# Performance work log

Hardware: AMD Instinct MI355X
Metric: run time of the kernel (lower is better)

Reference implementation:

```python
import jax, jax.numpy as jnp
import numpy as np

MASK_VALUE = -1000000.0  # matches torch sequence_mask fill value


def setup_inputs() -> dict:
    key = jax.random.key(0)
    k1, k2, k3, k4 = jax.random.split(key, 4)
    B, Tq, Tk, d = 16, 2048, 2048, 128
    queries = jax.random.normal(k1, (B, Tq, d), dtype=jnp.float32)
    keys = jax.random.normal(k2, (B, Tk, d), dtype=jnp.float32)
    values = jax.random.normal(k3, (B, Tk, d), dtype=jnp.float32)
    valid_lens = jax.random.randint(k4, (B, Tq), 0, Tk, dtype=jnp.int64)
    return {"queries": queries, "keys": keys, "values": values,
            "valid_lens": valid_lens}


def reference(queries, keys, values, valid_lens):
    d = queries.shape[-1]
    Tk = keys.shape[1]
    # scores: [B, Tq, Tk]
    scores = jnp.einsum('bqd,bkd->bqk', queries, keys) / jnp.sqrt(
        jnp.asarray(d, dtype=queries.dtype))
    # per-row length mask: position k is valid iff k < valid_lens[b, q]
    mask = jnp.arange(Tk)[None, None, :] < valid_lens[:, :, None]
    scores = jnp.where(mask, scores, jnp.asarray(MASK_VALUE, scores.dtype))
    attn = jax.nn.softmax(scores, axis=-1)
    # dropout p=0.0 -> identity
    return jnp.einsum('bqk,bkd->bqd', attn, values)
```

## Files before the change

### kernel.cpp

```cpp
#include <hip/hip_runtime.h>
#include <stdint.h>
#include <math.h>

#define NB 16
#define TQ 2048
#define TK 2048
#define DH 128

#define QK_STR 136
#define VT_STR 72
#define P_STR  72

typedef __attribute__((ext_vector_type(8))) short bf16x8;
typedef __attribute__((ext_vector_type(4))) float f32x4;
typedef __attribute__((ext_vector_type(8))) unsigned short u16x8;

__device__ __forceinline__ unsigned short f2b(float f) {
  union { float f; uint32_t u; } v; v.f = f;
  uint32_t u = v.u;
  return (unsigned short)((u + 0x7fffu + ((u >> 16) & 1u)) >> 16);
}

__device__ __forceinline__ u16x8 cvt8(const float* p) {
  const f32x4 a = *(const f32x4*)p;
  const f32x4 b = *(const f32x4*)(p + 4);
  u16x8 o;
#pragma unroll
  for (int j = 0; j < 4; ++j) { o[j] = f2b(a[j]); o[4 + j] = f2b(b[j]); }
  return o;
}

__global__ __launch_bounds__(256) void prep_kernel(const float* __restrict__ K,
                                                   const float* __restrict__ V,
                                                   unsigned short* __restrict__ Kb,
                                                   unsigned short* __restrict__ Vt) {
  __shared__ alignas(16) unsigned short tile[64][136];
  const int t = threadIdx.x;
  const int b = blockIdx.y;
  const int k0 = blockIdx.x * 64;

  const float* Ks = K + ((size_t)b * TK + k0) * DH;
  unsigned short* Kd = Kb + ((size_t)b * TK + k0) * DH;
#pragma unroll
  for (int i = 0; i < 4; ++i) {
    const int row = i * 16 + (t >> 4);
    const int c0 = (t & 15) * 8;
    *(u16x8*)(Kd + (size_t)row * DH + c0) = cvt8(Ks + (size_t)row * DH + c0);
  }
  const float* Vs = V + ((size_t)b * TK + k0) * DH;
#pragma unroll
  for (int i = 0; i < 4; ++i) {
    const int row = i * 16 + (t >> 4);
    const int c0 = (t & 15) * 8;
    *(u16x8*)(&tile[row][c0]) = cvt8(Vs + (size_t)row * DH + c0);
  }
  __syncthreads();
  {
    const int d = t & 127;
    const int kg = t >> 7;
    alignas(16) unsigned short tmp[32];
#pragma unroll
    for (int j = 0; j < 32; ++j) tmp[j] = tile[kg * 32 + j][d];
    unsigned short* dst = Vt + ((size_t)b * DH + d) * TK + k0 + kg * 32;
#pragma unroll
    for (int j = 0; j < 4; ++j)
      *(u16x8*)(dst + j * 8) = *(const u16x8*)(&tmp[j * 8]);
  }
}

template <bool USE_WS>
__global__ __launch_bounds__(256) void attn_kernel(const float* __restrict__ Q,
                                                   const void* __restrict__ Kp,
                                                   const void* __restrict__ Vp,
                                                   const int* __restrict__ vlen,
                                                   float* __restrict__ out) {
  __shared__ alignas(16) char smem[53248];
  __shared__ int s_bvl[4];
  unsigned short* sQ = (unsigned short*)smem;
  unsigned short* sK = (unsigned short*)(smem + 17408);
  unsigned short* sV = (unsigned short*)(smem + 34816);

  const int tid  = threadIdx.x;
  const int w    = tid >> 6;
  const int lane = tid & 63;
  const int quad = lane >> 4;
  const int l15  = lane & 15;
  const int b    = blockIdx.y;
  const int q0   = blockIdx.x * 64;

  const float* Qb = Q + ((size_t)b * TQ + q0) * DH;

#pragma unroll
  for (int i = 0; i < 4; ++i) {
    const int row = i * 16 + (tid >> 4);
    const int c0 = (tid & 15) * 8;
    *(u16x8*)(sQ + row * QK_STR + c0) = cvt8(Qb + (size_t)row * DH + c0);
  }

  int hw = 0;
#pragma unroll
  for (int i = 0; i < 8; ++i) hw |= vlen[2 * i + 1];
  const bool is64 = (hw == 0);

  const int qw = q0 + w * 16;
  int vlr[4];
#pragma unroll
  for (int r = 0; r < 4; ++r) {
    const int idx = b * TQ + qw + quad * 4 + r;
    int v = is64 ? vlen[2 * idx] : vlen[idx];
    v = (v < 0) ? 0 : ((v > TK) ? TK : v);
    vlr[r] = v;
  }
  int wvl = 0;
#pragma unroll
  for (int r = 0; r < 4; ++r) {
    const int e = (vlr[r] == 0) ? TK : vlr[r];
    wvl = max(wvl, e);
  }
  wvl = max(wvl, __shfl_xor(wvl, 16, 64));
  wvl = max(wvl, __shfl_xor(wvl, 32, 64));
  if (lane == 0) s_bvl[w] = wvl;

  __syncthreads();

  const int bvl = max(max(s_bvl[0], s_bvl[1]), max(s_bvl[2], s_bvl[3]));
  const int nt = (bvl + 63) >> 6;

  bf16x8 qa[4];
  {
    const unsigned short* qrow = sQ + (w * 16 + l15) * QK_STR;
#pragma unroll
    for (int kc = 0; kc < 4; ++kc)
      qa[kc] = *(const bf16x8*)(qrow + (kc * 4 + quad) * 8);
  }

  unsigned short* sP = (unsigned short*)smem + w * (16 * P_STR);

  f32x4 Of[8] = {};
  const float kScaleL2 = 0.08838834764831845f * 1.4426950408889634f;
  const float kMaskL2  = -1000000.0f * 1.4426950408889634f;
  float m_r[4], l_r[4];
#pragma unroll
  for (int r = 0; r < 4; ++r) { m_r[r] = -2.0e9f; l_r[r] = 0.f; }

  for (int t = 0; t < nt; ++t) {
    const int k0 = t * 64;
    __syncthreads();
    if (USE_WS) {
      const unsigned short* Kb = (const unsigned short*)Kp + (size_t)b * TK * DH;
      const unsigned short* Vb = (const unsigned short*)Vp + (size_t)b * DH * TK;
#pragma unroll
      for (int i = 0; i < 4; ++i) {
        const int row = i * 16 + (tid >> 4);
        const int ch = tid & 15;
        const u16x8 v = *(const u16x8*)(Kb + (size_t)(k0 + row) * DH + ch * 8);
        *(u16x8*)(sK + row * QK_STR + ch * 8) = v;
      }
#pragma unroll
      for (int i = 0; i < 4; ++i) {
        const int d = i * 32 + (tid >> 3);
        const int ch = tid & 7;
        const u16x8 v = *(const u16x8*)(Vb + (size_t)d * TK + k0 + ch * 8);
        *(u16x8*)(sV + d * VT_STR + ch * 8) = v;
      }
    } else {
      const float* Kb = (const float*)Kp + (size_t)b * TK * DH;
      const float* Vb = (const float*)Vp + (size_t)b * TK * DH;
#pragma unroll
      for (int i = 0; i < 4; ++i) {
        const int row = i * 16 + (tid >> 4);
        const int c0 = (tid & 15) * 8;
        *(u16x8*)(sK + row * QK_STR + c0) = cvt8(Kb + (size_t)(k0 + row) * DH + c0);
      }
#pragma unroll
      for (int i = 0; i < 4; ++i) {
        const int row = i * 16 + (tid >> 4);
        const int c0 = (tid & 15) * 8;
        *(u16x8*)(sV + row * QK_STR + c0) = cvt8(Vb + (size_t)(k0 + row) * DH + c0);
      }
    }
    __syncthreads();

    if (k0 >= wvl) continue;

    f32x4 sc[4] = {};
#pragma unroll
    for (int ct = 0; ct < 4; ++ct) {
      const unsigned short* kr = sK + (ct * 16 + l15) * QK_STR;
#pragma unroll
      for (int kc = 0; kc < 4; ++kc) {
        const bf16x8 kf = *(const bf16x8*)(kr + (kc * 4 + quad) * 8);
        sc[ct] = __builtin_amdgcn_mfma_f32_16x16x32_bf16(qa[kc], kf, sc[ct], 0, 0, 0);
      }
    }

    float ps[4][4];
    float tm[4] = {kMaskL2, kMaskL2, kMaskL2, kMaskL2};
#pragma unroll
    for (int ct = 0; ct < 4; ++ct) {
      const int kpos = k0 + ct * 16 + l15;
#pragma unroll
      for (int r = 0; r < 4; ++r) {
        const float s = (kpos < vlr[r]) ? sc[ct][r] * kScaleL2 : kMaskL2;
        ps[ct][r] = s;
        tm[r] = fmaxf(tm[r], s);
      }
    }
#pragma unroll
    for (int off = 1; off <= 8; off <<= 1)
#pragma unroll
      for (int r = 0; r < 4; ++r)
        tm[r] = fmaxf(tm[r], __shfl_xor(tm[r], off, 64));

#pragma unroll
    for (int r = 0; r < 4; ++r) {
      const float mn = fmaxf(m_r[r], tm[r]);
      const float al = exp2f(m_r[r] - mn);
      m_r[r] = mn;
      l_r[r] *= al;
#pragma unroll
      for (int dt = 0; dt < 8; ++dt) Of[dt][r] = Of[dt][r] * al;
    }

    float rs[4] = {0.f, 0.f, 0.f, 0.f};
    unsigned short pb[4][4];
#pragma unroll
    for (int ct = 0; ct < 4; ++ct)
#pragma unroll
      for (int r = 0; r < 4; ++r) {
        const float p = exp2f(ps[ct][r] - m_r[r]);
        rs[r] += p;
        pb[ct][r] = f2b(p);
      }
#pragma unroll
    for (int off = 1; off <= 8; off <<= 1)
#pragma unroll
      for (int r = 0; r < 4; ++r)
        rs[r] += __shfl_xor(rs[r], off, 64);
#pragma unroll
    for (int r = 0; r < 4; ++r) l_r[r] += rs[r];

#pragma unroll
    for (int ct = 0; ct < 4; ++ct)
#pragma unroll
      for (int r = 0; r < 4; ++r)
        sP[(quad * 4 + r) * P_STR + ct * 16 + l15] = pb[ct][r];
    __asm__ __volatile__("" ::: "memory");

    bf16x8 pa[2];
    {
      const unsigned short* pr = sP + l15 * P_STR;
#pragma unroll
      for (int ch = 0; ch < 2; ++ch)
        pa[ch] = *(const bf16x8*)(pr + (ch * 4 + quad) * 8);
    }

    if (USE_WS) {
#pragma unroll
      for (int dt = 0; dt < 8; ++dt) {
        const unsigned short* vr = sV + (dt * 16 + l15) * VT_STR;
#pragma unroll
        for (int ch = 0; ch < 2; ++ch) {
          const bf16x8 vf = *(const bf16x8*)(vr + (ch * 4 + quad) * 8);
          Of[dt] = __builtin_amdgcn_mfma_f32_16x16x32_bf16(pa[ch], vf, Of[dt], 0, 0, 0);
        }
      }
    } else {
#pragma unroll
      for (int dt = 0; dt < 8; ++dt) {
        const int col = dt * 16 + l15;
#pragma unroll
        for (int ch = 0; ch < 2; ++ch) {
          bf16x8 vf;
#pragma unroll
          for (int j = 0; j < 8; ++j) {
            const int k = ch * 32 + quad * 8 + j;
            vf[j] = ((const short*)sV)[k * QK_STR + col];
          }
          Of[dt] = __builtin_amdgcn_mfma_f32_16x16x32_bf16(pa[ch], vf, Of[dt], 0, 0, 0);
        }
      }
    }
  }

#pragma unroll
  for (int r = 0; r < 4; ++r) {
    const float inv = 1.0f / l_r[r];
    const int q = qw + quad * 4 + r;
    float* orow = out + ((size_t)b * TQ + q) * DH;
#pragma unroll
    for (int dt = 0; dt < 8; ++dt)
      orow[dt * 16 + l15] = Of[dt][r] * inv;
  }
}

extern "C" void kernel_launch(void* const* d_in, const int* in_sizes, int n_in,
                              void* d_out, int out_size, void* d_ws, size_t ws_size,
                              hipStream_t stream) {
  const float* Q = (const float*)d_in[0];
  const float* K = (const float*)d_in[1];
  const float* V = (const float*)d_in[2];
  const int* vl  = (const int*)d_in[3];
  float* out     = (float*)d_out;

  const size_t kb = (size_t)NB * TK * DH;
  if (ws_size >= kb * 2 * 2) {
    unsigned short* Kb = (unsigned short*)d_ws;
    unsigned short* Vt = Kb + kb;
    prep_kernel<<<dim3(TK / 64, NB), 256, 0, stream>>>(K, V, Kb, Vt);
    attn_kernel<true><<<dim3(TQ / 64, NB), 256, 0, stream>>>(Q, Kb, Vt, vl, out);
  } else {
    attn_kernel<false><<<dim3(TQ / 64, NB), 256, 0, stream>>>(Q, K, V, vl, out);
  }
}
```

Baseline: 194.0 us.

## Prefetch next K/V tile into registers and tile-contiguous V transpose layout

The prep kernel now writes transposed V as contiguous per-64-key tiles, so each attention tile load is one linear chunk instead of strided rows. The attention kernel prefetches the next K and V tiles into registers while computing the current tile, overlapping global loads with the MFMA work. It also skips the rescale of the output accumulator when no row's running max grows. The cost is more registers per thread, which may lower occupancy.

```diff
diff --git a/kernel.cpp b/kernel.cpp
--- a/kernel.cpp
+++ b/kernel.cpp
@@ -6,6 +6,7 @@
 #define TQ 2048
 #define TK 2048
 #define DH 128
+#define KT (TK / 64)
 
 #define QK_STR 136
 #define VT_STR 72
@@ -37,7 +38,8 @@
   __shared__ alignas(16) unsigned short tile[64][136];
   const int t = threadIdx.x;
   const int b = blockIdx.y;
-  const int k0 = blockIdx.x * 64;
+  const int kt = blockIdx.x;
+  const int k0 = kt * 64;
 
   const float* Ks = K + ((size_t)b * TK + k0) * DH;
   unsigned short* Kd = Kb + ((size_t)b * TK + k0) * DH;
@@ -56,24 +58,23 @@
   }
   __syncthreads();
   {
-    const int d = t & 127;
-    const int kg = t >> 7;
+    const int d = t >> 1;
+    const int half = t & 1;
     alignas(16) unsigned short tmp[32];
 #pragma unroll
-    for (int j = 0; j < 32; ++j) tmp[j] = tile[kg * 32 + j][d];
-    unsigned short* dst = Vt + ((size_t)b * DH + d) * TK + k0 + kg * 32;
+    for (int j = 0; j < 32; ++j) tmp[j] = tile[half * 32 + j][d];
+    unsigned short* dst = Vt + ((size_t)(b * KT + kt) * DH + d) * 64 + half * 32;
 #pragma unroll
     for (int j = 0; j < 4; ++j)
       *(u16x8*)(dst + j * 8) = *(const u16x8*)(&tmp[j * 8]);
   }
 }
 
-template <bool USE_WS>
-__global__ __launch_bounds__(256) void attn_kernel(const float* __restrict__ Q,
-                                                   const void* __restrict__ Kp,
-                                                   const void* __restrict__ Vp,
-                                                   const int* __restrict__ vlen,
-                                                   float* __restrict__ out) {
+__global__ __launch_bounds__(256) void attn_ws(const float* __restrict__ Q,
+                                               const unsigned short* __restrict__ Kp,
+                                               const unsigned short* __restrict__ Vp,
+                                               const int* __restrict__ vlen,
+                                               float* __restrict__ out) {
   __shared__ alignas(16) char smem[53248];
   __shared__ int s_bvl[4];
   unsigned short* sQ = (unsigned short*)smem;
@@ -89,7 +90,6 @@
   const int q0   = blockIdx.x * 64;
 
   const float* Qb = Q + ((size_t)b * TQ + q0) * DH;
-
 #pragma unroll
   for (int i = 0; i < 4; ++i) {
     const int row = i * 16 + (tid >> 4);
@@ -122,7 +122,6 @@
   if (lane == 0) s_bvl[w] = wvl;
 
   __syncthreads();
-
   const int bvl = max(max(s_bvl[0], s_bvl[1]), max(s_bvl[2], s_bvl[3]));
   const int nt = (bvl + 63) >> 6;
 
@@ -133,7 +132,6 @@
     for (int kc = 0; kc < 4; ++kc)
       qa[kc] = *(const bf16x8*)(qrow + (kc * 4 + quad) * 8);
   }
-
   unsigned short* sP = (unsigned short*)smem + w * (16 * P_STR);
 
   f32x4 Of[8] = {};
@@ -143,44 +141,236 @@
 #pragma unroll
   for (int r = 0; r < 4; ++r) { m_r[r] = -2.0e9f; l_r[r] = 0.f; }
 
+  const unsigned short* Kbase = Kp + (size_t)b * TK * DH;
+  const unsigned short* Vbase = Vp + (size_t)(b * KT) * DH * 64;
+  const int krow = tid >> 4;
+  const int kch  = tid & 15;
+
+  u16x8 kreg[4], vreg[4];
+  {
+    const unsigned short* Ksrc = Kbase;
+#pragma unroll
+    for (int i = 0; i < 4; ++i)
+      kreg[i] = *(const u16x8*)(Ksrc + (size_t)(i * 16 + krow) * DH + kch * 8);
+#pragma unroll
+    for (int i = 0; i < 4; ++i)
+      vreg[i] = *(const u16x8*)(Vbase + (i * 256 + tid) * 8);
+  }
+
+  for (int t = 0; t < nt; ++t) {
+#pragma unroll
+    for (int i = 0; i < 4; ++i)
+      *(u16x8*)(sK + (i * 16 + krow) * QK_STR + kch * 8) = kreg[i];
+#pragma unroll
+    for (int i = 0; i < 4; ++i) {
+      const int chunk = i * 256 + tid;
+      *(u16x8*)(sV + (chunk >> 3) * VT_STR + (chunk & 7) * 8) = vreg[i];
+    }
+    __syncthreads();
+
+    if (t + 1 < nt) {
+      const unsigned short* Ksrc = Kbase + (size_t)(t + 1) * 64 * DH;
+#pragma unroll
+      for (int i = 0; i < 4; ++i)
+        kreg[i] = *(const u16x8*)(Ksrc + (size_t)(i * 16 + krow) * DH + kch * 8);
+      const unsigned short* Vsrc = Vbase + (size_t)(t + 1) * (DH * 64);
+#pragma unroll
+      for (int i = 0; i < 4; ++i)
+        vreg[i] = *(const u16x8*)(Vsrc + (i * 256 + tid) * 8);
+    }
+
+    const int k0 = t * 64;
+    if (k0 < wvl) {
+      f32x4 sc[4] = {};
+#pragma unroll
+      for (int ct = 0; ct < 4; ++ct) {
+        const unsigned short* kr = sK + (ct * 16 + l15) * QK_STR;
+#pragma unroll
+        for (int kc = 0; kc < 4; ++kc) {
+          const bf16x8 kf = *(const bf16x8*)(kr + (kc * 4 + quad) * 8);
+          sc[ct] = __builtin_amdgcn_mfma_f32_16x16x32_bf16(qa[kc], kf, sc[ct], 0, 0, 0);
+        }
+      }
+
+      float ps[4][4];
+      float tm[4] = {kMaskL2, kMaskL2, kMaskL2, kMaskL2};
+#pragma unroll
+      for (int ct = 0; ct < 4; ++ct) {
+        const int kpos = k0 + ct * 16 + l15;
+#pragma unroll
+        for (int r = 0; r < 4; ++r) {
+          const float s = (kpos < vlr[r]) ? sc[ct][r] * kScaleL2 : kMaskL2;
+          ps[ct][r] = s;
+          tm[r] = fmaxf(tm[r], s);
+        }
+      }
+#pragma unroll
+      for (int off = 1; off <= 8; off <<= 1)
+#pragma unroll
+        for (int r = 0; r < 4; ++r)
+          tm[r] = fmaxf(tm[r], __shfl_xor(tm[r], off, 64));
+
+      bool anynew = false;
+#pragma unroll
+      for (int r = 0; r < 4; ++r) anynew = anynew || (tm[r] > m_r[r]);
+      if (__any((int)anynew)) {
+#pragma unroll
+        for (int r = 0; r < 4; ++r) {
+          const float mn = fmaxf(m_r[r], tm[r]);
+          const float al = exp2f(m_r[r] - mn);
+          m_r[r] = mn;
+          l_r[r] *= al;
+#pragma unroll
+          for (int dt = 0; dt < 8; ++dt) Of[dt][r] = Of[dt][r] * al;
+        }
+      }
+
+      float rs[4] = {0.f, 0.f, 0.f, 0.f};
+      unsigned short pb[4][4];
+#pragma unroll
+      for (int ct = 0; ct < 4; ++ct)
+#pragma unroll
+        for (int r = 0; r < 4; ++r) {
+          const float p = exp2f(ps[ct][r] - m_r[r]);
+          rs[r] += p;
+          pb[ct][r] = f2b(p);
+        }
+#pragma unroll
+      for (int off = 1; off <= 8; off <<= 1)
+#pragma unroll
+        for (int r = 0; r < 4; ++r)
+          rs[r] += __shfl_xor(rs[r], off, 64);
+#pragma unroll
+      for (int r = 0; r < 4; ++r) l_r[r] += rs[r];
+
+#pragma unroll
+      for (int ct = 0; ct < 4; ++ct)
+#pragma unroll
+        for (int r = 0; r < 4; ++r)
+          sP[(quad * 4 + r) * P_STR + ct * 16 + l15] = pb[ct][r];
+      __asm__ __volatile__("" ::: "memory");
+
+      bf16x8 pa[2];
+      {
+        const unsigned short* pr = sP + l15 * P_STR;
+#pragma unroll
+        for (int ch = 0; ch < 2; ++ch)
+          pa[ch] = *(const bf16x8*)(pr + (ch * 4 + quad) * 8);
+      }
+
+#pragma unroll
+      for (int dt = 0; dt < 8; ++dt) {
+        const unsigned short* vr = sV + (dt * 16 + l15) * VT_STR;
+#pragma unroll
+        for (int ch = 0; ch < 2; ++ch) {
+          const bf16x8 vf = *(const bf16x8*)(vr + (ch * 4 + quad) * 8);
+          Of[dt] = __builtin_amdgcn_mfma_f32_16x16x32_bf16(pa[ch], vf, Of[dt], 0, 0, 0);
+        }
+      }
+    }
+    __syncthreads();
+  }
+
+#pragma unroll
+  for (int r = 0; r < 4; ++r) {
+    const float inv = 1.0f / l_r[r];
+    const int q = qw + quad * 4 + r;
+    float* orow = out + ((size_t)b * TQ + q) * DH;
+#pragma unroll
+    for (int dt = 0; dt < 8; ++dt)
+      orow[dt * 16 + l15] = Of[dt][r] * inv;
+  }
+}
+
+__global__ __launch_bounds__(256) void attn_fb(const float* __restrict__ Q,
+                                               const float* __restrict__ Kp,
+                                               const float* __restrict__ Vp,
+                                               const int* __restrict__ vlen,
+                                               float* __restrict__ out) {
+  __shared__ alignas(16) char smem[53248];
+  __shared__ int s_bvl[4];
+  unsigned short* sQ = (unsigned short*)smem;
+  unsigned short* sK = (unsigned short*)(smem + 17408);
+  unsigned short* sV = (unsigned short*)(smem + 34816);
+
+  const int tid  = threadIdx.x;
+  const int w    = tid >> 6;
+  const int lane = tid & 63;
+  const int quad = lane >> 4;
+  const int l15  = lane & 15;
+  const int b    = blockIdx.y;
+  const int q0   = blockIdx.x * 64;
+
+  const float* Qb = Q + ((size_t)b * TQ + q0) * DH;
+#pragma unroll
+  for (int i = 0; i < 4; ++i) {
+    const int row = i * 16 + (tid >> 4);
+    const int c0 = (tid & 15) * 8;
+    *(u16x8*)(sQ + row * QK_STR + c0) = cvt8(Qb + (size_t)row * DH + c0);
+  }
+
+  int hw = 0;
+#pragma unroll
+  for (int i = 0; i < 8; ++i) hw |= vlen[2 * i + 1];
+  const bool is64 = (hw == 0);
+
+  const int qw = q0 + w * 16;
+  int vlr[4];
+#pragma unroll
+  for (int r = 0; r < 4; ++r) {
+    const int idx = b * TQ + qw + quad * 4 + r;
+    int v = is64 ? vlen[2 * idx] : vlen[idx];
+    v = (v < 0) ? 0 : ((v > TK) ? TK : v);
+    vlr[r] = v;
+  }
+  int wvl = 0;
+#pragma unroll
+  for (int r = 0; r < 4; ++r) {
+    const int e = (vlr[r] == 0) ? TK : vlr[r];
+    wvl = max(wvl, e);
+  }
+  wvl = max(wvl, __shfl_xor(wvl, 16, 64));
+  wvl = max(wvl, __shfl_xor(wvl, 32, 64));
+  if (lane == 0) s_bvl[w] = wvl;
+  __syncthreads();
+  const int bvl = max(max(s_bvl[0], s_bvl[1]), max(s_bvl[2], s_bvl[3]));
+  const int nt = (bvl + 63) >> 6;
+
+  bf16x8 qa[4];
+  {
+    const unsigned short* qrow = sQ + (w * 16 + l15) * QK_STR;
+#pragma unroll
+    for (int kc = 0; kc < 4; ++kc)
+      qa[kc] = *(const bf16x8*)(qrow + (kc * 4 + quad) * 8);
+  }
+  unsigned short* sP = (unsigned short*)smem + w * (16 * P_STR);
+
+  f32x4 Of[8] = {};
+  const float kScaleL2 = 0.08838834764831845f * 1.4426950408889634f;
+  const float kMaskL2  = -1000000.0f * 1.4426950408889634f;
+  float m_r[4], l_r[4];
+#pragma unroll
+  for (int r = 0; r < 4; ++r) { m_r[r] = -2.0e9f; l_r[r] = 0.f; }
+
+  const float* Kb = Kp + (size_t)b * TK * DH;
+  const float* Vb = Vp + (size_t)b * TK * DH;
+
   for (int t = 0; t < nt; ++t) {
     const int k0 = t * 64;
     __syncthreads();
-    if (USE_WS) {
-      const unsigned short* Kb = (const unsigned short*)Kp + (size_t)b * TK * DH;
-      const unsigned short* Vb = (const unsigned short*)Vp + (size_t)b * DH * TK;
-#pragma unroll
-      for (int i = 0; i < 4; ++i) {
-        const int row = i * 16 + (tid >> 4);
-        const int ch = tid & 15;
-        const u16x8 v = *(const u16x8*)(Kb + (size_t)(k0 + row) * DH + ch * 8);
-        *(u16x8*)(sK + row * QK_STR + ch * 8) = v;
-      }
-#pragma unroll
-      for (int i = 0; i < 4; ++i) {
-        const int d = i * 32 + (tid >> 3);
-        const int ch = tid & 7;
-        const u16x8 v = *(const u16x8*)(Vb + (size_t)d * TK + k0 + ch * 8);
-        *(u16x8*)(sV + d * VT_STR + ch * 8) = v;
-      }
-    } else {
-      const float* Kb = (const float*)Kp + (size_t)b * TK * DH;
-      const float* Vb = (const float*)Vp + (size_t)b * TK * DH;
-#pragma unroll
-      for (int i = 0; i < 4; ++i) {
-        const int row = i * 16 + (tid >> 4);
-        const int c0 = (tid & 15) * 8;
-        *(u16x8*)(sK + row * QK_STR + c0) = cvt8(Kb + (size_t)(k0 + row) * DH + c0);
-      }
-#pragma unroll
-      for (int i = 0; i < 4; ++i) {
-        const int row = i * 16 + (tid >> 4);
-        const int c0 = (tid & 15) * 8;
-        *(u16x8*)(sV + row * QK_STR + c0) = cvt8(Vb + (size_t)(k0 + row) * DH + c0);
-      }
+#pragma unroll
+    for (int i = 0; i < 4; ++i) {
+      const int row = i * 16 + (tid >> 4);
+      const int c0 = (tid & 15) * 8;
+      *(u16x8*)(sK + row * QK_STR + c0) = cvt8(Kb + (size_t)(k0 + row) * DH + c0);
+    }
+#pragma unroll
+    for (int i = 0; i < 4; ++i) {
+      const int row = i * 16 + (tid >> 4);
+      const int c0 = (tid & 15) * 8;
+      *(u16x8*)(sV + row * QK_STR + c0) = cvt8(Vb + (size_t)(k0 + row) * DH + c0);
     }
     __syncthreads();
-
     if (k0 >= wvl) continue;
 
     f32x4 sc[4] = {};
@@ -193,7 +383,6 @@
         sc[ct] = __builtin_amdgcn_mfma_f32_16x16x32_bf16(qa[kc], kf, sc[ct], 0, 0, 0);
       }
     }
-
     float ps[4][4];
     float tm[4] = {kMaskL2, kMaskL2, kMaskL2, kMaskL2};
 #pragma unroll
@@ -211,7 +400,6 @@
 #pragma unroll
       for (int r = 0; r < 4; ++r)
         tm[r] = fmaxf(tm[r], __shfl_xor(tm[r], off, 64));
-
 #pragma unroll
     for (int r = 0; r < 4; ++r) {
       const float mn = fmaxf(m_r[r], tm[r]);
@@ -221,7 +409,6 @@
 #pragma unroll
       for (int dt = 0; dt < 8; ++dt) Of[dt][r] = Of[dt][r] * al;
     }
-
     float rs[4] = {0.f, 0.f, 0.f, 0.f};
     unsigned short pb[4][4];
 #pragma unroll
@@ -239,14 +426,12 @@
         rs[r] += __shfl_xor(rs[r], off, 64);
 #pragma unroll
     for (int r = 0; r < 4; ++r) l_r[r] += rs[r];
-
 #pragma unroll
     for (int ct = 0; ct < 4; ++ct)
 #pragma unroll
       for (int r = 0; r < 4; ++r)
         sP[(quad * 4 + r) * P_STR + ct * 16 + l15] = pb[ct][r];
     __asm__ __volatile__("" ::: "memory");
-
     bf16x8 pa[2];
     {
       const unsigned short* pr = sP + l15 * P_STR;
@@ -254,35 +439,21 @@
       for (int ch = 0; ch < 2; ++ch)
         pa[ch] = *(const bf16x8*)(pr + (ch * 4 + quad) * 8);
     }
-
-    if (USE_WS) {
-#pragma unroll
-      for (int dt = 0; dt < 8; ++dt) {
-        const unsigned short* vr = sV + (dt * 16 + l15) * VT_STR;
-#pragma unroll
-        for (int ch = 0; ch < 2; ++ch) {
-          const bf16x8 vf = *(const bf16x8*)(vr + (ch * 4 + quad) * 8);
-          Of[dt] = __builtin_amdgcn_mfma_f32_16x16x32_bf16(pa[ch], vf, Of[dt], 0, 0, 0);
-        }
-      }
-    } else {
-#pragma unroll
-      for (int dt = 0; dt < 8; ++dt) {
-        const int col = dt * 16 + l15;
-#pragma unroll
-        for (int ch = 0; ch < 2; ++ch) {
-          bf16x8 vf;
-#pragma unroll
-          for (int j = 0; j < 8; ++j) {
-            const int k = ch * 32 + quad * 8 + j;
-            vf[j] = ((const short*)sV)[k * QK_STR + col];
-          }
-          Of[dt] = __builtin_amdgcn_mfma_f32_16x16x32_bf16(pa[ch], vf, Of[dt], 0, 0, 0);
-        }
-      }
-    }
-  }
-
+#pragma unroll
+    for (int dt = 0; dt < 8; ++dt) {
+      const int col = dt * 16 + l15;
+#pragma unroll
+      for (int ch = 0; ch < 2; ++ch) {
+        bf16x8 vf;
+#pragma unroll
+        for (int j = 0; j < 8; ++j) {
+          const int k = ch * 32 + quad * 8 + j;
+          vf[j] = ((const short*)sV)[k * QK_STR + col];
+        }
+        Of[dt] = __builtin_amdgcn_mfma_f32_16x16x32_bf16(pa[ch], vf, Of[dt], 0, 0, 0);
+      }
+    }
+  }
 #pragma unroll
   for (int r = 0; r < 4; ++r) {
     const float inv = 1.0f / l_r[r];
@@ -307,9 +478,9 @@
   if (ws_size >= kb * 2 * 2) {
     unsigned short* Kb = (unsigned short*)d_ws;
     unsigned short* Vt = Kb + kb;
-    prep_kernel<<<dim3(TK / 64, NB), 256, 0, stream>>>(K, V, Kb, Vt);
-    attn_kernel<true><<<dim3(TQ / 64, NB), 256, 0, stream>>>(Q, Kb, Vt, vl, out);
+    prep_kernel<<<dim3(KT, NB), 256, 0, stream>>>(K, V, Kb, Vt);
+    attn_ws<<<dim3(TQ / 64, NB), 256, 0, stream>>>(Q, Kb, Vt, vl, out);
   } else {
-    attn_kernel<false><<<dim3(TQ / 64, NB), 256, 0, stream>>>(Q, K, V, vl, out);
-  }
-}
+    attn_fb<<<dim3(TQ / 64, NB), 256, 0, stream>>>(Q, K, V, vl, out);
+  }
+}
```

Result: no change. 190.6 us (-1.8%).
